# Optimization experiments

Hardware: AMD Instinct MI355X
Metric: run time of the kernel (lower is better)

The kernel has to match this reference:

```python
import jax, jax.numpy as jnp
import numpy as np

B, S, E, ND = 4, 2048, 1024, 2


def setup_inputs() -> dict:
    key = jax.random.key(0)
    ks = jax.random.split(key, 10)
    def lin_w(k, out_f, in_f):
        return (jax.random.normal(k, (out_f, in_f), jnp.float32) / np.sqrt(in_f).astype(np.float32))
    inp = {}
    inp["x"] = jax.random.normal(ks[0], (B, S, E), jnp.float32)
    inp["tfidf_scores"] = jax.random.uniform(ks[1], (B, S), jnp.float32)
    names = ["q_f", "k_f", "v_f", "q_b", "k_b", "v_b"]
    for i, n in enumerate(names):
        inp["W" + n] = lin_w(ks[2 + i], ND * E, E)
        inp["b" + n] = jnp.zeros((ND * E,), jnp.float32)
    inp["Wo"] = lin_w(ks[8], E, ND * E)
    inp["bo"] = jnp.zeros((E,), jnp.float32)
    return inp


def _proj(x, W, b):
    # Linear(E -> ND*E) then reshape to (B, S, ND, E)
    y = jnp.einsum('bse,fe->bsf', x, W) + b
    return y.reshape(x.shape[0], x.shape[1], ND, E)


def _attend(q, k, v, tfidf):
    # q,k,v: (B, S, ND, E); tfidf: (B, S) weights keys
    scale = 1.0 / jnp.sqrt(jnp.asarray(E, q.dtype))
    scores = jnp.einsum('bsde,btde->bdst', q, k) * scale
    scores = scores * tfidf[:, None, None, :]
    attn = jax.nn.softmax(scores, axis=-1)
    return jnp.einsum('bdst,btde->bsde', attn, v)


def reference(x, tfidf_scores, Wq_f, bq_f, Wk_f, bk_f, Wv_f, bv_f,
              Wq_b, bq_b, Wk_b, bk_b, Wv_b, bv_b, Wo, bo):
    # forward direction
    qf = _proj(x, Wq_f, bq_f)
    kf = _proj(x, Wk_f, bk_f)
    vf = _proj(x, Wv_f, bv_f)
    out_f = _attend(qf, kf, vf, tfidf_scores)
    # backward direction: reversed sequence
    xr = x[:, ::-1]
    tr = tfidf_scores[:, ::-1]
    qb = _proj(xr, Wq_b, bq_b)
    kb = _proj(xr, Wk_b, bk_b)
    vb = _proj(xr, Wv_b, bv_b)
    out_b = _attend(qb, kb, vb, tr)[:, ::-1]
    comb = (out_f + out_b).reshape(x.shape[0], x.shape[1], ND * E)
    return jnp.einsum('bsf,ef->bse', comb, Wo) + bo
```

## Files before the change

kernel.cpp:

```cpp
#include <hip/hip_runtime.h>
#include <hip/hip_bf16.h>
#include <stdint.h>

#define SEQ 2048
#define EMB 1024

typedef __attribute__((ext_vector_type(4))) float f32x4;
typedef __attribute__((ext_vector_type(8))) __bf16 bf16x8v;
typedef __attribute__((ext_vector_type(8))) unsigned short u16x8;
typedef __attribute__((ext_vector_type(4))) unsigned short u16x4;

static __device__ __forceinline__ float bf2f(unsigned short u){
  union { unsigned int i; float f; } v; v.i = ((unsigned int)u) << 16; return v.f;
}
static __device__ __forceinline__ unsigned short f2bf(float f){
  union { float f; unsigned int i; } v; v.f = f;
  unsigned int r = v.i + 0x7FFFu + ((v.i >> 16) & 1u);
  return (unsigned short)(r >> 16);
}

static __device__ __forceinline__ void gload16(const unsigned short* g, unsigned short* l){
  __builtin_amdgcn_global_load_lds(
      (__attribute__((address_space(1))) unsigned int*)(g),
      (__attribute__((address_space(3))) unsigned int*)(l), 16, 0, 0);
}

static __device__ __forceinline__ int xcd_swz(int bid, int nwg){
  int q = nwg >> 3;
  return (bid & 7) * q + (bid >> 3);
}

__global__ __launch_bounds__(256) void k_cvt_bf16(const float* __restrict__ in,
                                                  unsigned short* __restrict__ out, long n4){
  long i = (long)blockIdx.x * 256 + threadIdx.x;
  if (i >= n4) return;
  float4 v = ((const float4*)in)[i];
  u16x4 o; o.x = f2bf(v.x); o.y = f2bf(v.y); o.z = f2bf(v.z); o.w = f2bf(v.w);
  ((u16x4*)out)[i] = o;
}

__global__ __launch_bounds__(256) void k_build_wcat(
    const float* __restrict__ w0, const float* __restrict__ w1,
    const float* __restrict__ w2, const float* __restrict__ w3,
    const float* __restrict__ w4, const float* __restrict__ w5,
    unsigned short* __restrict__ wcat){
  long i = (long)blockIdx.x * 256 + threadIdx.x;
  long g = i * 4;
  int m = (int)(g >> 21);
  const float* src = (m==0)?w0:(m==1)?w1:(m==2)?w2:(m==3)?w3:(m==4)?w4:w5;
  long loc = g & ((1L<<21)-1);
  float4 v = *(const float4*)&src[loc];
  u16x4 o; o.x=f2bf(v.x); o.y=f2bf(v.y); o.z=f2bf(v.z); o.w=f2bf(v.w);
  *(u16x4*)&wcat[g] = o;
}

__global__ __launch_bounds__(256) void k_build_bcat(
    const float* b0, const float* b1, const float* b2,
    const float* b3, const float* b4, const float* b5, float* __restrict__ bcat){
  int i = blockIdx.x * 256 + threadIdx.x;
  int m = i >> 11;
  const float* src = (m==0)?b0:(m==1)?b1:(m==2)?b2:(m==3)?b3:(m==4)?b4:b5;
  bcat[i] = src[i & 2047];
}

#define M_LIN   0
#define M_SCORE 1
#define M_PV    2
#define M_OUT   3

template<int MODE, int BN>
__global__ __launch_bounds__(512, 2)
void gemm4p(const unsigned short* __restrict__ A_,
            const unsigned short* __restrict__ B_,
            unsigned short* __restrict__ Cb, float* __restrict__ Cf,
            const float* __restrict__ bias, const float* __restrict__ tfb,
            int ld, int ldc, int tilesN, int accflag)
{
  constexpr int KD  = (MODE==M_PV || MODE==M_OUT) ? 2048 : 1024;
  constexpr int NT  = KD/64;
  constexpr int NREP= BN/64;
  constexpr int NLO = NREP/2;
  constexpr int LB  = BN/128;

  __shared__ __attribute__((aligned(16))) unsigned short As[2][256*64];
  __shared__ __attribute__((aligned(16))) unsigned short Bs[2][BN*64];

  const int tid = threadIdx.x;
  const int lane = tid & 63, wid = tid >> 6;
  const int wr = wid >> 2, wc = wid & 3;

  const int tile = xcd_swz(blockIdx.x, gridDim.x);
  const int tm = tile / tilesN, tn = tile % tilesN;
  const int y  = blockIdx.y;

  const unsigned short *A0 = A_, *B0 = B_;
  unsigned short* Cbp = Cb;
  float* Cfp = Cf;
  const float* trow = nullptr;

  if constexpr (MODE==M_SCORE) {
    const int bl = y >> 1, d = y & 1;
    A0 = A_ + (size_t)bl*SEQ*ld + d*1024;
    B0 = A0 + 2048;
    Cbp = Cb + (size_t)y*SEQ*SEQ;
    trow = tfb + (size_t)bl*SEQ;
  } else if constexpr (MODE==M_PV) {
    A0 = A_ + (size_t)y*SEQ*SEQ;
    B0 = B_ + (size_t)y*EMB*SEQ;
    Cbp = Cb + (size_t)(y>>1)*SEQ*2048 + (y&1)*1024;
  }

  const int sr = tid >> 3, ss = tid & 7;
  const int swz = (ss ^ (sr & 7)) * 8;
  const long tmrow = (long)tm*256, tncol = (long)tn*BN;
  const int lrow = lane & 15, lks = lane >> 4;

  const unsigned short* gA = A0 + (size_t)(tmrow + sr)*ld + swz;
  const unsigned short* gB = B0 + (size_t)(tncol + sr)*ld + swz;

  f32x4 acc[8][NREP];
  #pragma unroll
  for (int m=0;m<8;++m)
    #pragma unroll
    for (int n=0;n<NREP;++n)
      #pragma unroll
      for (int r=0;r<4;++r) acc[m][n][r] = 0.f;

#define SA_H(b_, h_, t_) { \
    const long ko_ = (long)(t_)*64; \
    _Pragma("unroll") \
    for (int p=0;p<2;++p){ \
      const int p2_ = (h_)*2 + p; \
      gload16(gA + (size_t)(p2_*64)*ld + ko_, &As[b_][p2_*4096 + tid*8]); \
    } }

#define SB_H(b_, h_, t_) { \
    const long ko_ = (long)(t_)*64; \
    _Pragma("unroll") \
    for (int p=0;p<LB;++p){ \
      const int p2_ = (h_)*LB + p; \
      gload16(gB + (size_t)(p2_*64)*ld + ko_, &Bs[b_][p2_*4096 + tid*8]); \
    } }

#define LDA_F(dst, b_, mh) { \
    _Pragma("unroll") \
    for (int m=0;m<4;++m){ \
      int row_ = (m + 4*(mh))*32 + wr*16 + lrow; \
      _Pragma("unroll") \
      for (int kk=0;kk<2;++kk){ \
        int slot_ = (kk*4 + lks) ^ (row_ & 7); \
        dst[m*2+kk] = *(const bf16x8v*)&As[b_][row_*64 + slot_*8]; \
      } } }

#define LDB_F(dst, b_, nh) { \
    _Pragma("unroll") \
    for (int n=0;n<NLO;++n){ \
      int row_ = (n + NLO*(nh))*64 + wc*16 + lrow; \
      _Pragma("unroll") \
      for (int kk=0;kk<2;++kk){ \
        int slot_ = (kk*4 + lks) ^ (row_ & 7); \
        dst[n*2+kk] = *(const bf16x8v*)&Bs[b_][row_*64 + slot_*8]; \
      } } }

#define MMAC(mh, bfrag, nh) { \
    __builtin_amdgcn_s_setprio(1); \
    _Pragma("unroll") \
    for (int m=0;m<4;++m) \
      _Pragma("unroll") \
      for (int n=0;n<NLO;++n) \
        _Pragma("unroll") \
        for (int kk=0;kk<2;++kk) \
          acc[(mh)*4+m][(nh)*NLO+n] = __builtin_amdgcn_mfma_f32_16x16x32_bf16( \
              aF[m*2+kk], bfrag[n*2+kk], acc[(mh)*4+m][(nh)*NLO+n], 0,0,0); \
    __builtin_amdgcn_s_setprio(0); }

#define GATEN(N_) { \
    asm volatile("s_waitcnt vmcnt(" #N_ ")" ::: "memory"); \
    __builtin_amdgcn_sched_barrier(0); \
    __builtin_amdgcn_s_barrier(); \
    __builtin_amdgcn_sched_barrier(0); }

  SA_H(0,0,0); SB_H(0,0,0); SB_H(0,1,0); SA_H(0,1,0);

  bf16x8v aF[8], bL[2*NLO], bH[2*NLO];

  for (int t = 0; t < NT-1; ++t) {
    const int b_ = t & 1, nb_ = b_ ^ 1;
    SA_H(nb_,0,t+1);
    if constexpr (LB==2) { GATEN(6) } else { GATEN(5) }
    LDA_F(aF, b_, 0);
    LDB_F(bL, b_, 0);
    MMAC(0, bL, 0);
    SB_H(nb_,0,t+1);
    if constexpr (LB==2) { GATEN(6) } else { GATEN(5) }
    LDB_F(bH, b_, 1);
    MMAC(0, bH, 1);
    SB_H(nb_,1,t+1);
    if constexpr (LB==2) { GATEN(6) } else { GATEN(4) }
    LDA_F(aF, b_, 1);
    MMAC(1, bH, 1);
    SA_H(nb_,1,t+1);
    MMAC(1, bL, 0);
  }

  {
    const int b_ = (NT-1) & 1;
    if constexpr (LB==2) { GATEN(4) } else { GATEN(3) }
    LDA_F(aF, b_, 0);
    LDB_F(bL, b_, 0);
    MMAC(0, bL, 0);
    GATEN(2)
    LDB_F(bH, b_, 1);
    MMAC(0, bH, 1);
    GATEN(0)
    LDA_F(aF, b_, 1);
    MMAC(1, bH, 1);
    MMAC(1, bL, 0);
  }

  const int rr = (lane >> 4) * 4, cc = lane & 15;
  #pragma unroll
  for (int n=0;n<NREP;++n) {
    const long col = tncol + n*64 + wc*16 + cc;
    float cmul = 1.f, cadd = 0.f;
    if constexpr (MODE==M_SCORE) cmul = 0.03125f * trow[col];
    if constexpr (MODE==M_LIN || MODE==M_OUT) cadd = bias[col];
    #pragma unroll
    for (int m=0;m<8;++m) {
      const long row = tmrow + m*32 + wr*16 + rr;
      #pragma unroll
      for (int r=0;r<4;++r) {
        float v = acc[m][n][r];
        if constexpr (MODE==M_SCORE) v *= cmul;
        else v += cadd;
        if constexpr (MODE==M_OUT) {
          Cfp[(row + r)*(size_t)ldc + col] = v;
        } else if constexpr (MODE==M_PV) {
          size_t idx = (row + r)*(size_t)ldc + col;
          float w = v + (accflag ? bf2f(Cbp[idx]) : 0.f);
          Cbp[idx] = f2bf(w);
        } else {
          Cbp[(row + r)*(size_t)ldc + col] = f2bf(v);
        }
      }
    }
  }
#undef SA_H
#undef SB_H
#undef LDA_F
#undef LDB_F
#undef MMAC
#undef GATEN
}

__global__ __launch_bounds__(256) void k_softmax(unsigned short* __restrict__ Sc){
  long row = blockIdx.x;
  unsigned short* p = Sc + row*SEQ + threadIdx.x*8;
  u16x8 raw = *(const u16x8*)p;
  float v[8]; float mx = -3.0e38f;
  #pragma unroll
  for (int j=0;j<8;++j){ v[j] = bf2f(raw[j]); mx = fmaxf(mx, v[j]); }
  #pragma unroll
  for (int o=1;o<64;o<<=1) mx = fmaxf(mx, __shfl_xor(mx, o));
  __shared__ float redm[4], reds[4];
  int wid = threadIdx.x >> 6, lane = threadIdx.x & 63;
  if (lane == 0) redm[wid] = mx;
  __syncthreads();
  mx = fmaxf(fmaxf(redm[0],redm[1]), fmaxf(redm[2],redm[3]));
  float s = 0.f;
  #pragma unroll
  for (int j=0;j<8;++j){ v[j] = __expf(v[j]-mx); s += v[j]; }
  #pragma unroll
  for (int o=1;o<64;o<<=1) s += __shfl_xor(s, o);
  if (lane == 0) reds[wid] = s;
  __syncthreads();
  s = reds[0]+reds[1]+reds[2]+reds[3];
  float inv = 1.0f / s;
  u16x8 outv;
  #pragma unroll
  for (int j=0;j<8;++j) outv[j] = f2bf(v[j]*inv);
  *(u16x8*)p = outv;
}

__global__ __launch_bounds__(256) void k_transpose_v(const unsigned short* __restrict__ Vsrc,
                                                     unsigned short* __restrict__ VT, int ld){
  __shared__ unsigned short tile[64][72];
  int y = blockIdx.y; int bl = y >> 1, d = y & 1;
  int tt = (blockIdx.x & 31) * 64;
  int te = (blockIdx.x >> 5) * 64;
  const unsigned short* src = Vsrc + (size_t)bl*SEQ*ld + d*1024;
  int tid = threadIdx.x;
  #pragma unroll
  for (int it=0; it<2; ++it){
    int c = it*256 + tid;
    int r = c >> 3, c8 = (c & 7) * 8;
    u16x8 v = *(const u16x8*)&src[(size_t)(tt + r)*ld + te + c8];
    *(u16x8*)&tile[r][c8] = v;
  }
  __syncthreads();
  #pragma unroll
  for (int it=0; it<2; ++it){
    int c = it*256 + tid;
    int re = c >> 3, c8 = (c & 7) * 8;
    u16x8 o;
    #pragma unroll
    for (int j=0;j<8;++j) o[j] = tile[c8 + j][re];
    *(u16x8*)&VT[((size_t)y*EMB + te + re)*SEQ + tt + c8] = o;
  }
}

extern "C" void kernel_launch(void* const* d_in, const int* in_sizes, int n_in,
                              void* d_out, int out_size, void* d_ws, size_t ws_size,
                              hipStream_t stream){
  const float* x  = (const float*)d_in[0];
  const float* tf = (const float*)d_in[1];
  const float* W[6]; const float* bz[6];
  for (int i=0;i<6;++i){ W[i]=(const float*)d_in[2+2*i]; bz[i]=(const float*)d_in[3+2*i]; }
  const float* Wo = (const float*)d_in[14];
  const float* bo = (const float*)d_in[15];
  float* outp = (float*)d_out;

  auto al = [](size_t b){ return (b + 255) & ~(size_t)255; };
  const size_t SZ_XB   = (size_t)8192*1024*2;
  const size_t SZ_WCAT = (size_t)12288*1024*2;
  const size_t SZ_WOB  = (size_t)1024*2048*2;
  const size_t SZ_BCAT = (size_t)12288*4;
  const size_t SZ_AO   = (size_t)8192*2048*2;
  const size_t fixedB  = al(SZ_XB)+al(SZ_WCAT)+al(SZ_WOB)+al(SZ_BCAT)+al(SZ_AO);

  auto chB = [&](int CB, bool merged)->size_t {
    return al((size_t)CB*SEQ*(merged?12288:6144)*2)
         + al((size_t)CB*2*SEQ*SEQ*2)
         + al((size_t)CB*2*EMB*SEQ*2);
  };
  int CB; bool merged;
  if      (ws_size >= fixedB + chB(2,true))  { CB=2; merged=true;  }
  else if (ws_size >= fixedB + chB(2,false)) { CB=2; merged=false; }
  else if (ws_size >= fixedB + chB(1,false)) { CB=1; merged=false; }
  else return;
  const int ldY = merged ? 12288 : 6144;

  char* ws = (char*)d_ws; size_t off = 0;
  auto take = [&](size_t bytes)->char* { char* p = ws + off; off += al(bytes); return p; };
  unsigned short* xb   = (unsigned short*)take(SZ_XB);
  unsigned short* Wcat = (unsigned short*)take(SZ_WCAT);
  unsigned short* WoB  = (unsigned short*)take(SZ_WOB);
  float*          bcat = (float*)take(SZ_BCAT);
  unsigned short* AO   = (unsigned short*)take(SZ_AO);
  unsigned short* Ych  = (unsigned short*)take((size_t)CB*SEQ*ldY*2);
  unsigned short* Sc   = (unsigned short*)take((size_t)CB*2*SEQ*SEQ*2);
  unsigned short* VT   = (unsigned short*)take((size_t)CB*2*EMB*SEQ*2);

  k_cvt_bf16   <<<8192, 256, 0, stream>>>(x, xb, 2097152);
  k_build_wcat <<<12288,256, 0, stream>>>(W[0],W[1],W[2],W[3],W[4],W[5], Wcat);
  k_cvt_bf16   <<<2048, 256, 0, stream>>>(Wo, WoB, 524288);
  k_build_bcat <<<48,   256, 0, stream>>>(bz[0],bz[1],bz[2],bz[3],bz[4],bz[5], bcat);

  for (int c = 0; c < 4/CB; ++c) {
    const int b0 = c*CB;
    const unsigned short* xchunk = xb + (size_t)b0*SEQ*1024;
    if (merged) {
      gemm4p<M_LIN,256><<<dim3(CB*8*48, 1), 512, 0, stream>>>(
          xchunk, Wcat, Ych, nullptr, bcat, nullptr, 1024, 12288, 48, 0);
    }
    for (int dir = 0; dir < 2; ++dir) {
      const unsigned short* Ybase = Ych + (merged ? dir*6144 : 0);
      if (!merged) {
        gemm4p<M_LIN,256><<<dim3(CB*8*24, 1), 512, 0, stream>>>(
            xchunk, Wcat + (size_t)dir*6144*1024, Ych, nullptr,
            bcat + dir*6144, nullptr, 1024, 6144, 24, 0);
      }
      gemm4p<M_SCORE,256><<<dim3(64, 2*CB), 512, 0, stream>>>(
          Ybase, nullptr, Sc, nullptr, nullptr, tf + (size_t)b0*SEQ,
          ldY, 2048, 8, 0);
      k_softmax    <<<2*CB*SEQ, 256, 0, stream>>>(Sc);
      k_transpose_v<<<dim3(512, 2*CB), 256, 0, stream>>>(Ybase + 4096, VT, ldY);
      gemm4p<M_PV,128><<<dim3(64, 2*CB), 512, 0, stream>>>(
          Sc, VT, AO + (size_t)b0*SEQ*2048, nullptr, nullptr, nullptr,
          2048, 2048, 8, dir);
    }
  }
  gemm4p<M_OUT,128><<<dim3(256, 1), 512, 0, stream>>>(
      AO, WoB, nullptr, outp, bo, nullptr, 2048, 1024, 8, 0);
}
```

Measured before the change: 761.9 us.

## Fuse softmax into score and PV GEMM epilogues, batch both directions per launch

The score GEMM epilogue now exponentiates the scaled scores directly without max subtraction, stores the unnormalized values, and accumulates row sums with atomics. The PV GEMM divides by those row sums, so the separate softmax kernel and its full read/write pass over the score matrix are removed. Both directions (and up to all 4 batches when workspace allows) are launched in one grid via blockIdx.z. The main loop is also re-pipelined so fragment loads for the next k-step are issued before the MMA tail. Skipping the max subtraction risks overflow if scores get large, atomics add contention, and the larger workspace configuration needs more memory.

```diff
diff --git a/kernel.cpp b/kernel.cpp
--- a/kernel.cpp
+++ b/kernel.cpp
@@ -96,18 +96,22 @@
   const unsigned short *A0 = A_, *B0 = B_;
   unsigned short* Cbp = Cb;
   float* Cfp = Cf;
+  float* rsp = nullptr;
   const float* trow = nullptr;
+  const float* rsd = nullptr;
 
   if constexpr (MODE==M_SCORE) {
     const int bl = y >> 1, d = y & 1;
-    A0 = A_ + (size_t)bl*SEQ*ld + d*1024;
+    A0 = A_ + (size_t)bl*SEQ*ld + (size_t)blockIdx.z*6144 + d*1024;
     B0 = A0 + 2048;
-    Cbp = Cb + (size_t)y*SEQ*SEQ;
+    Cbp = Cb + ((size_t)blockIdx.z*gridDim.y + y)*SEQ*SEQ;
+    rsp = Cf + ((size_t)blockIdx.z*gridDim.y + y)*SEQ;
     trow = tfb + (size_t)bl*SEQ;
   } else if constexpr (MODE==M_PV) {
     A0 = A_ + (size_t)y*SEQ*SEQ;
     B0 = B_ + (size_t)y*EMB*SEQ;
     Cbp = Cb + (size_t)(y>>1)*SEQ*2048 + (y&1)*1024;
+    rsd = tfb + (size_t)y*SEQ;
   }
 
   const int sr = tid >> 3, ss = tid & 7;
@@ -180,67 +184,120 @@
     __builtin_amdgcn_s_barrier(); \
     __builtin_amdgcn_sched_barrier(0); }
 
+#define SBAR() __builtin_amdgcn_sched_barrier(0);
+
+  bf16x8v aF[8], bL[2*NLO], bH[2*NLO];
+
   SA_H(0,0,0); SB_H(0,0,0); SB_H(0,1,0); SA_H(0,1,0);
-
-  bf16x8v aF[8], bL[2*NLO], bH[2*NLO];
+  if constexpr (LB==2) { GATEN(4) } else { GATEN(3) }
+  LDA_F(aF, 0, 0);
+  LDB_F(bL, 0, 0);
+  SBAR()
 
   for (int t = 0; t < NT-1; ++t) {
     const int b_ = t & 1, nb_ = b_ ^ 1;
     SA_H(nb_,0,t+1);
-    if constexpr (LB==2) { GATEN(6) } else { GATEN(5) }
-    LDA_F(aF, b_, 0);
-    LDB_F(bL, b_, 0);
+    GATEN(4)
+    LDB_F(bH, b_, 1);
+    SBAR()
     MMAC(0, bL, 0);
     SB_H(nb_,0,t+1);
-    if constexpr (LB==2) { GATEN(6) } else { GATEN(5) }
-    LDB_F(bH, b_, 1);
+    if constexpr (LB==2) { GATEN(4) } else { GATEN(3) }
     MMAC(0, bH, 1);
+    LDA_F(aF, b_, 1);
+    SBAR()
     SB_H(nb_,1,t+1);
-    if constexpr (LB==2) { GATEN(6) } else { GATEN(4) }
-    LDA_F(aF, b_, 1);
     MMAC(1, bH, 1);
     SA_H(nb_,1,t+1);
+    if constexpr (LB==2) { GATEN(4) } else { GATEN(3) }
     MMAC(1, bL, 0);
+    LDA_F(aF, nb_, 0);
+    LDB_F(bL, nb_, 0);
+    SBAR()
   }
 
   {
     const int b_ = (NT-1) & 1;
-    if constexpr (LB==2) { GATEN(4) } else { GATEN(3) }
-    LDA_F(aF, b_, 0);
-    LDB_F(bL, b_, 0);
-    MMAC(0, bL, 0);
     GATEN(2)
     LDB_F(bH, b_, 1);
+    SBAR()
+    MMAC(0, bL, 0);
+    GATEN(0)
     MMAC(0, bH, 1);
-    GATEN(0)
     LDA_F(aF, b_, 1);
+    SBAR()
     MMAC(1, bH, 1);
     MMAC(1, bL, 0);
   }
 
   const int rr = (lane >> 4) * 4, cc = lane & 15;
-  #pragma unroll
-  for (int n=0;n<NREP;++n) {
-    const long col = tncol + n*64 + wc*16 + cc;
-    float cmul = 1.f, cadd = 0.f;
-    if constexpr (MODE==M_SCORE) cmul = 0.03125f * trow[col];
-    if constexpr (MODE==M_LIN || MODE==M_OUT) cadd = bias[col];
-    #pragma unroll
-    for (int m=0;m<8;++m) {
-      const long row = tmrow + m*32 + wr*16 + rr;
-      #pragma unroll
-      for (int r=0;r<4;++r) {
-        float v = acc[m][n][r];
-        if constexpr (MODE==M_SCORE) v *= cmul;
-        else v += cadd;
-        if constexpr (MODE==M_OUT) {
-          Cfp[(row + r)*(size_t)ldc + col] = v;
-        } else if constexpr (MODE==M_PV) {
-          size_t idx = (row + r)*(size_t)ldc + col;
-          float w = v + (accflag ? bf2f(Cbp[idx]) : 0.f);
+
+  if constexpr (MODE==M_SCORE) {
+    float cm[NREP];
+    #pragma unroll
+    for (int n=0;n<NREP;++n) cm[n] = 0.03125f * trow[tncol + n*64 + wc*16 + cc];
+    #pragma unroll
+    for (int m=0;m<8;++m)
+      #pragma unroll
+      for (int n=0;n<NREP;++n)
+        #pragma unroll
+        for (int r=0;r<4;++r)
+          acc[m][n][r] = __expf(acc[m][n][r] * cm[n]);
+    #pragma unroll
+    for (int n=0;n<NREP;++n){
+      const long col = tncol + n*64 + wc*16 + cc;
+      #pragma unroll
+      for (int m=0;m<8;++m){
+        const long row = tmrow + m*32 + wr*16 + rr;
+        #pragma unroll
+        for (int r=0;r<4;++r)
+          Cbp[(row + r)*(size_t)ldc + col] = f2bf(acc[m][n][r]);
+      }
+    }
+    #pragma unroll
+    for (int m=0;m<8;++m){
+      #pragma unroll
+      for (int r=0;r<4;++r){
+        float s = 0.f;
+        #pragma unroll
+        for (int n=0;n<NREP;++n) s += acc[m][n][r];
+        s += __shfl_xor(s, 1); s += __shfl_xor(s, 2);
+        s += __shfl_xor(s, 4); s += __shfl_xor(s, 8);
+        if ((lane & 15) == 0)
+          atomicAdd(&rsp[tmrow + m*32 + wr*16 + rr + r], s);
+      }
+    }
+  } else if constexpr (MODE==M_PV) {
+    #pragma unroll
+    for (int m=0;m<8;++m){
+      const long row0 = tmrow + m*32 + wr*16 + rr;
+      float4 rsv = *(const float4*)&rsd[row0];
+      float inv[4];
+      inv[0] = 1.f/rsv.x; inv[1] = 1.f/rsv.y; inv[2] = 1.f/rsv.z; inv[3] = 1.f/rsv.w;
+      #pragma unroll
+      for (int n=0;n<NREP;++n){
+        const long col = tncol + n*64 + wc*16 + cc;
+        #pragma unroll
+        for (int r=0;r<4;++r){
+          size_t idx = (row0 + r)*(size_t)ldc + col;
+          float w = acc[m][n][r]*inv[r] + (accflag ? bf2f(Cbp[idx]) : 0.f);
           Cbp[idx] = f2bf(w);
-        } else {
-          Cbp[(row + r)*(size_t)ldc + col] = f2bf(v);
+        }
+      }
+    }
+  } else {
+    #pragma unroll
+    for (int n=0;n<NREP;++n){
+      const long col = tncol + n*64 + wc*16 + cc;
+      const float cadd = bias[col];
+      #pragma unroll
+      for (int m=0;m<8;++m){
+        const long row = tmrow + m*32 + wr*16 + rr;
+        #pragma unroll
+        for (int r=0;r<4;++r){
+          float v = acc[m][n][r] + cadd;
+          if constexpr (MODE==M_OUT) Cfp[(row + r)*(size_t)ldc + col] = v;
+          else                       Cbp[(row + r)*(size_t)ldc + col] = f2bf(v);
         }
       }
     }
@@ -251,44 +308,17 @@
 #undef LDB_F
 #undef MMAC
 #undef GATEN
-}
-
-__global__ __launch_bounds__(256) void k_softmax(unsigned short* __restrict__ Sc){
-  long row = blockIdx.x;
-  unsigned short* p = Sc + row*SEQ + threadIdx.x*8;
-  u16x8 raw = *(const u16x8*)p;
-  float v[8]; float mx = -3.0e38f;
-  #pragma unroll
-  for (int j=0;j<8;++j){ v[j] = bf2f(raw[j]); mx = fmaxf(mx, v[j]); }
-  #pragma unroll
-  for (int o=1;o<64;o<<=1) mx = fmaxf(mx, __shfl_xor(mx, o));
-  __shared__ float redm[4], reds[4];
-  int wid = threadIdx.x >> 6, lane = threadIdx.x & 63;
-  if (lane == 0) redm[wid] = mx;
-  __syncthreads();
-  mx = fmaxf(fmaxf(redm[0],redm[1]), fmaxf(redm[2],redm[3]));
-  float s = 0.f;
-  #pragma unroll
-  for (int j=0;j<8;++j){ v[j] = __expf(v[j]-mx); s += v[j]; }
-  #pragma unroll
-  for (int o=1;o<64;o<<=1) s += __shfl_xor(s, o);
-  if (lane == 0) reds[wid] = s;
-  __syncthreads();
-  s = reds[0]+reds[1]+reds[2]+reds[3];
-  float inv = 1.0f / s;
-  u16x8 outv;
-  #pragma unroll
-  for (int j=0;j<8;++j) outv[j] = f2bf(v[j]*inv);
-  *(u16x8*)p = outv;
+#undef SBAR
 }
 
 __global__ __launch_bounds__(256) void k_transpose_v(const unsigned short* __restrict__ Vsrc,
                                                      unsigned short* __restrict__ VT, int ld){
   __shared__ unsigned short tile[64][72];
-  int y = blockIdx.y; int bl = y >> 1, d = y & 1;
+  int yo = blockIdx.z*gridDim.y + blockIdx.y;
+  int bl = blockIdx.y >> 1, d = blockIdx.y & 1;
   int tt = (blockIdx.x & 31) * 64;
   int te = (blockIdx.x >> 5) * 64;
-  const unsigned short* src = Vsrc + (size_t)bl*SEQ*ld + d*1024;
+  const unsigned short* src = Vsrc + (size_t)bl*SEQ*ld + (size_t)blockIdx.z*6144 + d*1024;
   int tid = threadIdx.x;
   #pragma unroll
   for (int it=0; it<2; ++it){
@@ -305,7 +335,7 @@
     u16x8 o;
     #pragma unroll
     for (int j=0;j<8;++j) o[j] = tile[c8 + j][re];
-    *(u16x8*)&VT[((size_t)y*EMB + te + re)*SEQ + tt + c8] = o;
+    *(u16x8*)&VT[((size_t)yo*EMB + te + re)*SEQ + tt + c8] = o;
   }
 }
 
@@ -328,17 +358,22 @@
   const size_t SZ_AO   = (size_t)8192*2048*2;
   const size_t fixedB  = al(SZ_XB)+al(SZ_WCAT)+al(SZ_WOB)+al(SZ_BCAT)+al(SZ_AO);
 
-  auto chB = [&](int CB, bool merged)->size_t {
+  auto chB = [&](int CB, bool merged, bool both)->size_t {
+    int nd = both ? 2 : 1;
     return al((size_t)CB*SEQ*(merged?12288:6144)*2)
-         + al((size_t)CB*2*SEQ*SEQ*2)
-         + al((size_t)CB*2*EMB*SEQ*2);
+         + al((size_t)nd*CB*2*SEQ*SEQ*2)
+         + al((size_t)nd*CB*2*EMB*SEQ*2)
+         + al((size_t)nd*CB*2*SEQ*4);
   };
-  int CB; bool merged;
-  if      (ws_size >= fixedB + chB(2,true))  { CB=2; merged=true;  }
-  else if (ws_size >= fixedB + chB(2,false)) { CB=2; merged=false; }
-  else if (ws_size >= fixedB + chB(1,false)) { CB=1; merged=false; }
+  int CB; bool merged, both;
+  if      (ws_size >= fixedB + chB(4,true ,true )) { CB=4; merged=true;  both=true;  }
+  else if (ws_size >= fixedB + chB(2,true ,true )) { CB=2; merged=true;  both=true;  }
+  else if (ws_size >= fixedB + chB(2,true ,false)) { CB=2; merged=true;  both=false; }
+  else if (ws_size >= fixedB + chB(2,false,false)) { CB=2; merged=false; both=false; }
+  else if (ws_size >= fixedB + chB(1,false,false)) { CB=1; merged=false; both=false; }
   else return;
   const int ldY = merged ? 12288 : 6144;
+  const int nd = both ? 2 : 1;
 
   char* ws = (char*)d_ws; size_t off = 0;
   auto take = [&](size_t bytes)->char* { char* p = ws + off; off += al(bytes); return p; };
@@ -348,8 +383,12 @@
   float*          bcat = (float*)take(SZ_BCAT);
   unsigned short* AO   = (unsigned short*)take(SZ_AO);
   unsigned short* Ych  = (unsigned short*)take((size_t)CB*SEQ*ldY*2);
-  unsigned short* Sc   = (unsigned short*)take((size_t)CB*2*SEQ*SEQ*2);
-  unsigned short* VT   = (unsigned short*)take((size_t)CB*2*EMB*SEQ*2);
+  const size_t scHalf = (size_t)CB*2*SEQ*SEQ;
+  const size_t vtHalf = (size_t)CB*2*EMB*SEQ;
+  const size_t rsHalf = (size_t)CB*2*SEQ;
+  unsigned short* Sc = (unsigned short*)take(nd*scHalf*2);
+  unsigned short* VT = (unsigned short*)take(nd*vtHalf*2);
+  float*          rs = (float*)take(nd*rsHalf*4);
 
   k_cvt_bf16   <<<8192, 256, 0, stream>>>(x, xb, 2097152);
   k_build_wcat <<<12288,256, 0, stream>>>(W[0],W[1],W[2],W[3],W[4],W[5], Wcat);
@@ -363,21 +402,32 @@
       gemm4p<M_LIN,256><<<dim3(CB*8*48, 1), 512, 0, stream>>>(
           xchunk, Wcat, Ych, nullptr, bcat, nullptr, 1024, 12288, 48, 0);
     }
-    for (int dir = 0; dir < 2; ++dir) {
-      const unsigned short* Ybase = Ych + (merged ? dir*6144 : 0);
-      if (!merged) {
-        gemm4p<M_LIN,256><<<dim3(CB*8*24, 1), 512, 0, stream>>>(
-            xchunk, Wcat + (size_t)dir*6144*1024, Ych, nullptr,
-            bcat + dir*6144, nullptr, 1024, 6144, 24, 0);
-      }
-      gemm4p<M_SCORE,256><<<dim3(64, 2*CB), 512, 0, stream>>>(
-          Ybase, nullptr, Sc, nullptr, nullptr, tf + (size_t)b0*SEQ,
-          ldY, 2048, 8, 0);
-      k_softmax    <<<2*CB*SEQ, 256, 0, stream>>>(Sc);
-      k_transpose_v<<<dim3(512, 2*CB), 256, 0, stream>>>(Ybase + 4096, VT, ldY);
-      gemm4p<M_PV,128><<<dim3(64, 2*CB), 512, 0, stream>>>(
-          Sc, VT, AO + (size_t)b0*SEQ*2048, nullptr, nullptr, nullptr,
-          2048, 2048, 8, dir);
+    if (both) {
+      hipMemsetAsync(rs, 0, 2*rsHalf*4, stream);
+      gemm4p<M_SCORE,256><<<dim3(64, 2*CB, 2), 512, 0, stream>>>(
+          Ych, nullptr, Sc, rs, nullptr, tf + (size_t)b0*SEQ, ldY, 2048, 8, 0);
+      k_transpose_v<<<dim3(512, 2*CB, 2), 256, 0, stream>>>(Ych + 4096, VT, ldY);
+      for (int dir = 0; dir < 2; ++dir) {
+        gemm4p<M_PV,128><<<dim3(64, 2*CB), 512, 0, stream>>>(
+            Sc + dir*scHalf, VT + dir*vtHalf, AO + (size_t)b0*SEQ*2048, nullptr,
+            nullptr, rs + dir*rsHalf, 2048, 2048, 8, dir);
+      }
+    } else {
+      for (int dir = 0; dir < 2; ++dir) {
+        const unsigned short* Ybase = Ych + (merged ? dir*6144 : 0);
+        if (!merged) {
+          gemm4p<M_LIN,256><<<dim3(CB*8*24, 1), 512, 0, stream>>>(
+              xchunk, Wcat + (size_t)dir*6144*1024, Ych, nullptr,
+              bcat + dir*6144, nullptr, 1024, 6144, 24, 0);
+        }
+        hipMemsetAsync(rs, 0, rsHalf*4, stream);
+        gemm4p<M_SCORE,256><<<dim3(64, 2*CB, 1), 512, 0, stream>>>(
+            Ybase, nullptr, Sc, rs, nullptr, tf + (size_t)b0*SEQ, ldY, 2048, 8, 0);
+        k_transpose_v<<<dim3(512, 2*CB, 1), 256, 0, stream>>>(Ybase + 4096, VT, ldY);
+        gemm4p<M_PV,128><<<dim3(64, 2*CB), 512, 0, stream>>>(
+            Sc, VT, AO + (size_t)b0*SEQ*2048, nullptr,
+            nullptr, rs, 2048, 2048, 8, dir);
+      }
     }
   }
   gemm4p<M_OUT,128><<<dim3(256, 1), 512, 0, stream>>>(
```

Result: faster. 705.5 us, median of 2 (-7.4%).
